# Performance work log

Measured on AMD Instinct MI355X. Metric: run time of the kernel, lower is better.

Reference implementation:

```python
import jax, jax.numpy as jnp
import numpy as np

HID = 512
HEADS = 8
HEAD_DIM = HID // HEADS
B, S = 2, 4096


def setup_inputs() -> dict:
    key = jax.random.key(0)
    ks = jax.random.split(key, 11)
    sc = 0.02
    return {
        "query": jax.random.normal(ks[0], (B, S, HID), jnp.float32),
        "key": jax.random.normal(ks[1], (B, S, HID), jnp.float32),
        "value": jax.random.normal(ks[2], (B, S, HID), jnp.float32),
        "Wq": jax.random.normal(ks[3], (HID, HID), jnp.float32) * sc,
        "bq": jax.random.normal(ks[4], (HID,), jnp.float32) * sc,
        "Wk": jax.random.normal(ks[5], (HID, HID), jnp.float32) * sc,
        "bk": jax.random.normal(ks[6], (HID,), jnp.float32) * sc,
        "Wv": jax.random.normal(ks[7], (HID, HID), jnp.float32) * sc,
        "bv": jax.random.normal(ks[8], (HID,), jnp.float32) * sc,
        "Wo": jax.random.normal(ks[9], (HID, HID), jnp.float32) * sc,
        "bo": jax.random.normal(ks[10], (HID,), jnp.float32) * sc,
    }


def reference(query, key, value, Wq, bq, Wk, bk, Wv, bv, Wo, bo):
    b, s, _ = query.shape
    scale = jnp.sqrt(jnp.float32(HEAD_DIM))
    # projections (nn.Linear: x @ W.T + b)
    Q = query @ Wq.T + bq
    K = key @ Wk.T + bk
    V = value @ Wv.T + bv
    # split heads: [b, h, s, d]
    Q = Q.reshape(b, s, HEADS, HEAD_DIM).transpose(0, 2, 1, 3)
    K = K.reshape(b, s, HEADS, HEAD_DIM).transpose(0, 2, 1, 3)
    V = V.reshape(b, s, HEADS, HEAD_DIM).transpose(0, 2, 1, 3)
    # scaled dot-product attention (mask=None, dropout in eval mode = identity)
    energy = jnp.einsum('bhqd,bhkd->bhqk', Q, K) / scale
    attention = jax.nn.softmax(energy, axis=-1)
    x = jnp.einsum('bhqk,bhkd->bhqd', attention, V)
    x = x.transpose(0, 2, 1, 3).reshape(b, s, HID)
    return x @ Wo.T + bo
```

## Files before the change

kernel.cpp:

```cpp
#include <hip/hip_runtime.h>
#include <stdint.h>

#define HID 512
#define NH 8
#define HD 64
#define BATCH 2
#define SEQ 4096
#define M_TOT (BATCH*SEQ)
#define NBH (BATCH*NH)
#define SPLITK 4

typedef __attribute__((ext_vector_type(8))) short short8;
typedef __attribute__((ext_vector_type(4))) float floatx4;
typedef unsigned short u16;

__device__ inline u16 f2bf(float x) {
  unsigned u = __builtin_bit_cast(unsigned, x);
  unsigned r = u + 0x7fff + ((u >> 16) & 1);
  return (u16)(r >> 16);
}

__device__ inline float bf2f(u16 h) {
  unsigned u = ((unsigned)h) << 16;
  return __builtin_bit_cast(float, u);
}

__device__ inline unsigned cvt_pk_bf16(float a, float b) {
  unsigned r;
  asm("v_cvt_pk_bf16_f32 %0, %1, %2" : "=v"(r) : "v"(a), "v"(b));
  return r;
}

__device__ inline void gll16(const void* g, void* l) {
  __builtin_amdgcn_global_load_lds((const __attribute__((address_space(1))) void*)g,
                                   (__attribute__((address_space(3))) void*)l, 16, 0, 0);
}


__global__ void cvt_all(const float* __restrict__ q, const float* __restrict__ k,
                        const float* __restrict__ v, const float* __restrict__ wq,
                        const float* __restrict__ wk, const float* __restrict__ wv,
                        const float* __restrict__ wo,
                        u16* __restrict__ xq, u16* __restrict__ xk,
                        u16* __restrict__ xv, u16* __restrict__ wb) {
  const size_t NW = (size_t)HID * HID;
  int bx = (int)blockIdx.x;
  const float* src; u16* dst; int blk;
  if (bx < 12288) {
    int seg = bx >> 12;
    blk = bx & 4095;
    src = (seg == 0) ? q : ((seg == 1) ? k : v);
    dst = (seg == 0) ? xq : ((seg == 1) ? xk : xv);
  } else {
    int w = (bx - 12288) >> 8;
    blk = (bx - 12288) & 255;
    src = (w == 0) ? wq : ((w == 1) ? wk : ((w == 2) ? wv : wo));
    dst = wb + (size_t)w * NW;
  }
  int i = (blk * 256 + (int)threadIdx.x) * 4;
  const float4 val = *(const float4*)(src + i);
  union { uint2 u; u16 h[4]; } pk;
  pk.h[0] = f2bf(val.x); pk.h[1] = f2bf(val.y);
  pk.h[2] = f2bf(val.z); pk.h[3] = f2bf(val.w);
  *(uint2*)(dst + i) = pk.u;
}

__global__ __launch_bounds__(256) void gemm_qkv(
    const u16* __restrict__ Xq, const u16* __restrict__ Xk, const u16* __restrict__ Xv,
    const u16* __restrict__ Wb,
    const float* __restrict__ bq, const float* __restrict__ bk, const float* __restrict__ bv,
    u16* __restrict__ Qp, u16* __restrict__ Kp, u16* __restrict__ Vt) {
  const int z = blockIdx.z;
  const u16* X = (z == 0) ? Xq : ((z == 1) ? Xk : Xv);
  const u16* W = Wb + (size_t)z * (HID * HID);
  const float* bias = (z == 0) ? bq : ((z == 1) ? bk : bv);

  __shared__ u16 As[128 * 32];
  __shared__ u16 Bs[128 * 32];

  const int tid = threadIdx.x;
  const int wid = tid >> 6, lane = tid & 63;
  const int wm = wid >> 1, wn = wid & 1;
  const int quad = lane >> 4, l16 = lane & 15;
  const int m0 = (int)blockIdx.x * 128, n0 = (int)blockIdx.y * 128;
  const int srow = lane >> 2;
  const int scol = (lane & 3) * 8;

  floatx4 acc[4][4];
#pragma unroll
  for (int i = 0; i < 4; i++)
#pragma unroll
    for (int j = 0; j < 4; j++) acc[i][j] = floatx4{0.f, 0.f, 0.f, 0.f};

  for (int k0 = 0; k0 < HID; k0 += 32) {
#pragma unroll
    for (int r = 0; r < 2; r++) {
      int row = r * 64 + wid * 16 + srow;
      gll16(X + (size_t)(m0 + row) * HID + k0 + scol, &As[(r * 64 + wid * 16) * 32]);
      gll16(W + (size_t)(n0 + row) * HID + k0 + scol, &Bs[(r * 64 + wid * 16) * 32]);
    }
    __syncthreads();
    short8 af[4], bf[4];
#pragma unroll
    for (int mt = 0; mt < 4; mt++)
      af[mt] = *(const short8*)&As[(wm * 64 + mt * 16 + l16) * 32 + quad * 8];
#pragma unroll
    for (int nt = 0; nt < 4; nt++)
      bf[nt] = *(const short8*)&Bs[(wn * 64 + nt * 16 + l16) * 32 + quad * 8];
#pragma unroll
    for (int mt = 0; mt < 4; mt++)
#pragma unroll
      for (int nt = 0; nt < 4; nt++)
        acc[mt][nt] = __builtin_amdgcn_mfma_f32_16x16x32_bf16(af[mt], bf[nt], acc[mt][nt], 0, 0, 0);
    __syncthreads();
  }

#pragma unroll
  for (int mt = 0; mt < 4; mt++) {
#pragma unroll
    for (int nt = 0; nt < 4; nt++) {
      int ncol = n0 + wn * 64 + nt * 16 + l16;
      float bias_v = bias[ncol];
      int h = ncol >> 6, d = ncol & 63;
#pragma unroll
      for (int r = 0; r < 4; r++) {
        int mrow = m0 + wm * 64 + mt * 16 + quad * 4 + r;
        float v = acc[mt][nt][r] + bias_v;
        int b = mrow >> 12, s = mrow & (SEQ - 1);
        size_t base = (size_t)(b * NH + h) * SEQ * HD;
        if (z == 2) {
          int kk = ((s >> 2) & 3) * 8 + ((s >> 4) & 1) * 4 + (s & 3);
          size_t idx = base + (size_t)(s >> 5) * 2048 + (d >> 4) * 512
                     + (kk >> 3) * 128 + (d & 15) * 8 + (kk & 7);
          Vt[idx] = f2bf(v);
        } else {
          size_t idx = base + (size_t)(s >> 4) * 1024 + (d >> 3) * 128 + (s & 15) * 8 + (d & 7);
          if (z == 0) Qp[idx] = f2bf(v * 0.18033688f);
          else        Kp[idx] = f2bf(v);
        }
      }
    }
  }
}

__global__ __launch_bounds__(256) void gemm_out(
    const u16* __restrict__ X, const u16* __restrict__ W,
    const float* __restrict__ bias, float* __restrict__ out) {
  __shared__ u16 As[128 * 32];
  __shared__ u16 Bs[64 * 32];

  const int tid = threadIdx.x;
  const int wid = tid >> 6, lane = tid & 63;
  const int wm = wid >> 1, wn = wid & 1;
  const int quad = lane >> 4, l16 = lane & 15;
  const int m0 = (int)blockIdx.x * 128, n0 = (int)blockIdx.y * 64;
  const int srow = lane >> 2;
  const int scol = (lane & 3) * 8;

  floatx4 acc[4][2];
#pragma unroll
  for (int i = 0; i < 4; i++)
#pragma unroll
    for (int j = 0; j < 2; j++) acc[i][j] = floatx4{0.f, 0.f, 0.f, 0.f};

  for (int k0 = 0; k0 < HID; k0 += 32) {
#pragma unroll
    for (int r = 0; r < 2; r++) {
      int row = r * 64 + wid * 16 + srow;
      gll16(X + (size_t)(m0 + row) * HID + k0 + scol, &As[(r * 64 + wid * 16) * 32]);
    }
    {
      int row = wid * 16 + srow;
      gll16(W + (size_t)(n0 + row) * HID + k0 + scol, &Bs[(wid * 16) * 32]);
    }
    __syncthreads();
    short8 af[4], bf[2];
#pragma unroll
    for (int mt = 0; mt < 4; mt++)
      af[mt] = *(const short8*)&As[(wm * 64 + mt * 16 + l16) * 32 + quad * 8];
#pragma unroll
    for (int nt = 0; nt < 2; nt++)
      bf[nt] = *(const short8*)&Bs[(wn * 32 + nt * 16 + l16) * 32 + quad * 8];
#pragma unroll
    for (int mt = 0; mt < 4; mt++)
#pragma unroll
      for (int nt = 0; nt < 2; nt++)
        acc[mt][nt] = __builtin_amdgcn_mfma_f32_16x16x32_bf16(af[mt], bf[nt], acc[mt][nt], 0, 0, 0);
    __syncthreads();
  }

#pragma unroll
  for (int mt = 0; mt < 4; mt++) {
#pragma unroll
    for (int nt = 0; nt < 2; nt++) {
      int ncol = n0 + wn * 32 + nt * 16 + l16;
      float bias_v = bias[ncol];
#pragma unroll
      for (int r = 0; r < 4; r++) {
        int mrow = m0 + wm * 64 + mt * 16 + quad * 4 + r;
        out[(size_t)mrow * HID + ncol] = acc[mt][nt][r] + bias_v;
      }
    }
  }
}

__global__ __launch_bounds__(256) void attn_kernel(
    const u16* __restrict__ Qp, const u16* __restrict__ Kp,
    const u16* __restrict__ Vt, u16* __restrict__ Opb, float* __restrict__ Lp) {
  const int bh = blockIdx.y;
  const int sp = blockIdx.z;
  const int q0 = (int)blockIdx.x * 128;
  const u16* Qh = Qp + (size_t)bh * SEQ * HD;
  const u16* Kh = Kp + (size_t)bh * SEQ * HD;
  const u16* Vh = Vt + (size_t)bh * SEQ * HD;

  __shared__ u16 Ks[2][4096];
  __shared__ u16 Vs[2][4096];

  const int tid = threadIdx.x;
  const int wid = tid >> 6, lane = tid & 63;
  const int quad = lane >> 4, l16 = lane & 15;

  short8 qf[2][2];
#pragma unroll
  for (int kq = 0; kq < 2; kq++)
#pragma unroll
    for (int n = 0; n < 2; n++)
      qf[kq][n] = *(const short8*)(Qh + (size_t)(q0 / 16 + wid * 2 + n) * 1024 + (kq * 4 + quad) * 128 + l16 * 8);

  float l_part[2] = {0.f, 0.f};
  floatx4 o[2][4];
#pragma unroll
  for (int m = 0; m < 2; m++)
#pragma unroll
    for (int dt = 0; dt < 4; dt++) o[m][dt] = floatx4{0.f, 0.f, 0.f, 0.f};

  const int kv_lo = sp * (SEQ / SPLITK), kv_hi = kv_lo + SEQ / SPLITK;

  auto stage = [&](int buf, int kv0) {
    const u16* kg = Kh + (size_t)(kv0 >> 4) * 1024;
    const u16* vg = Vh + (size_t)(kv0 >> 4) * 1024;
#pragma unroll
    for (int r = 0; r < 2; r++) {
      int c = wid + r * 4;
      gll16(kg + c * 512 + lane * 8, &Ks[buf][c * 512]);
      gll16(vg + c * 512 + lane * 8, &Vs[buf][c * 512]);
    }
  };

  stage(0, kv_lo);
  __syncthreads();

  int ibuf = 0;
  for (int kv0 = kv_lo; kv0 < kv_hi; kv0 += 64) {
    if (kv0 + 64 < kv_hi) stage(ibuf ^ 1, kv0 + 64);

#pragma unroll
    for (int gg = 0; gg < 2; gg++) {
      const u16* Kb = &Ks[ibuf][gg * 2048];
      short8 akA0 = *(const short8*)&Kb[quad * 128 + l16 * 8];
      short8 akA1 = *(const short8*)&Kb[(4 + quad) * 128 + l16 * 8];
      short8 akB0 = *(const short8*)&Kb[1024 + quad * 128 + l16 * 8];
      short8 akB1 = *(const short8*)&Kb[1024 + (4 + quad) * 128 + l16 * 8];
      short8 vf[4];
#pragma unroll
      for (int dt = 0; dt < 4; dt++)
        vf[dt] = *(const short8*)&Vs[ibuf][gg * 2048 + dt * 512 + quad * 128 + l16 * 8];

      floatx4 stA[2], stB[2];
#pragma unroll
      for (int n = 0; n < 2; n++) {
        stA[n] = __builtin_amdgcn_mfma_f32_16x16x32_bf16(akA0, qf[0][n], floatx4{0.f,0.f,0.f,0.f}, 0, 0, 0);
        stB[n] = __builtin_amdgcn_mfma_f32_16x16x32_bf16(akB0, qf[0][n], floatx4{0.f,0.f,0.f,0.f}, 0, 0, 0);
        stA[n] = __builtin_amdgcn_mfma_f32_16x16x32_bf16(akA1, qf[1][n], stA[n], 0, 0, 0);
        stB[n] = __builtin_amdgcn_mfma_f32_16x16x32_bf16(akB1, qf[1][n], stB[n], 0, 0, 0);
      }

#pragma unroll
      for (int n = 0; n < 2; n++) {
        float a0 = __builtin_amdgcn_exp2f(stA[n][0]);
        float a1 = __builtin_amdgcn_exp2f(stA[n][1]);
        float a2 = __builtin_amdgcn_exp2f(stA[n][2]);
        float a3 = __builtin_amdgcn_exp2f(stA[n][3]);
        float b0 = __builtin_amdgcn_exp2f(stB[n][0]);
        float b1 = __builtin_amdgcn_exp2f(stB[n][1]);
        float b2 = __builtin_amdgcn_exp2f(stB[n][2]);
        float b3 = __builtin_amdgcn_exp2f(stB[n][3]);
        l_part[n] += ((a0 + a1) + (a2 + a3)) + ((b0 + b1) + (b2 + b3));
        union { unsigned u[4]; short8 s; } pk;
        pk.u[0] = cvt_pk_bf16(a0, a1);
        pk.u[1] = cvt_pk_bf16(a2, a3);
        pk.u[2] = cvt_pk_bf16(b0, b1);
        pk.u[3] = cvt_pk_bf16(b2, b3);
#pragma unroll
        for (int dt = 0; dt < 4; dt++)
          o[n][dt] = __builtin_amdgcn_mfma_f32_16x16x32_bf16(pk.s, vf[dt], o[n][dt], 0, 0, 0);
      }
    }
    __syncthreads();
    ibuf ^= 1;
  }

#pragma unroll
  for (int n = 0; n < 2; n++) {
    l_part[n] += __shfl_xor(l_part[n], 16);
    l_part[n] += __shfl_xor(l_part[n], 32);
  }
  u16* Oph = Opb + (size_t)(sp * NBH + bh) * SEQ * HD;
  float* Lph = Lp + (size_t)(sp * NBH + bh) * SEQ;
  if (quad == 0) {
#pragma unroll
    for (int n = 0; n < 2; n++)
      Lph[q0 + wid * 32 + n * 16 + l16] = l_part[n];
  }
#pragma unroll
  for (int m = 0; m < 2; m++) {
#pragma unroll
    for (int r = 0; r < 4; r++) {
      int s = q0 + wid * 32 + m * 16 + quad * 4 + r;
#pragma unroll
      for (int dt = 0; dt < 4; dt++)
        Oph[(size_t)s * HD + dt * 16 + l16] = f2bf(o[m][dt][r]);
    }
  }
}

__global__ __launch_bounds__(256) void combine_kernel(
    const u16* __restrict__ Opb, const float* __restrict__ Lp, u16* __restrict__ Xo) {
  int idx = (int)blockIdx.x * 256 + (int)threadIdx.x;
  int e = idx * 4;
  int bh = e >> 18;
  int rem = e & 262143;
  int q = rem >> 6, d = rem & 63;
  float acc0 = 0.f, acc1 = 0.f, acc2 = 0.f, acc3 = 0.f, lsum = 0.f;
#pragma unroll
  for (int sp = 0; sp < SPLITK; sp++) {
    size_t i = ((size_t)(sp * NBH + bh) * SEQ + q) * HD + d;
    union { uint2 u; u16 h[4]; } pk;
    pk.u = *(const uint2*)(Opb + i);
    acc0 += bf2f(pk.h[0]); acc1 += bf2f(pk.h[1]);
    acc2 += bf2f(pk.h[2]); acc3 += bf2f(pk.h[3]);
    lsum += Lp[(size_t)(sp * NBH + bh) * SEQ + q];
  }
  float inv = 1.f / lsum;
  int b = bh >> 3, h = bh & 7;
  u16* dst = Xo + ((size_t)(b * SEQ + q)) * HID + h * HD + d;
  union { uint2 u; u16 hh[4]; } pk;
  pk.hh[0] = f2bf(acc0 * inv);
  pk.hh[1] = f2bf(acc1 * inv);
  pk.hh[2] = f2bf(acc2 * inv);
  pk.hh[3] = f2bf(acc3 * inv);
  *(uint2*)dst = pk.u;
}

extern "C" void kernel_launch(void* const* d_in, const int* in_sizes, int n_in,
                              void* d_out, int out_size, void* d_ws, size_t ws_size,
                              hipStream_t stream) {
  const float* q  = (const float*)d_in[0];
  const float* k  = (const float*)d_in[1];
  const float* v  = (const float*)d_in[2];
  const float* Wq = (const float*)d_in[3];
  const float* bq = (const float*)d_in[4];
  const float* Wk = (const float*)d_in[5];
  const float* bk = (const float*)d_in[6];
  const float* Wv = (const float*)d_in[7];
  const float* bv = (const float*)d_in[8];
  const float* Wo = (const float*)d_in[9];
  const float* bo = (const float*)d_in[10];

  u16* wsb = (u16*)d_ws;
  const size_t NW = (size_t)HID * HID;
  const size_t NX = (size_t)M_TOT * HID;
  u16* Wb = wsb;
  u16* Xq = wsb + 4 * NW;
  u16* Xk = Xq + NX;
  u16* Xv = Xk + NX;
  u16* Qp = Xv + NX;
  u16* Kp = Qp + NX;
  u16* Vt = Kp + NX;
  u16* Xo = Vt + NX;
  u16* Opb = Xo + NX;
  float* Lp = (float*)(Opb + (size_t)SPLITK * NBH * SEQ * HD);

  dim3 blk(256);
  cvt_all<<<dim3(13312), blk, 0, stream>>>(q, k, v, Wq, Wk, Wv, Wo, Xq, Xk, Xv, Wb);

  gemm_qkv<<<dim3(64, 4, 3), blk, 0, stream>>>(Xq, Xk, Xv, Wb, bq, bk, bv, Qp, Kp, Vt);
  attn_kernel<<<dim3(32, NBH, SPLITK), blk, 0, stream>>>(Qp, Kp, Vt, Opb, Lp);
  combine_kernel<<<dim3(4096), blk, 0, stream>>>(Opb, Lp, Xo);
  gemm_out<<<dim3(64, 8), blk, 0, stream>>>(Xo, Wb + 3 * NW, bo, (float*)d_out);
}
```

Measured before the change: 234.3 us.

## Fuse activation bf16 conversion into QKV GEMM and split-K combine into output GEMM

The fp32 activations are no longer converted to bf16 in a separate pass. Instead the QKV GEMM loads fp32 rows and packs them to bf16 while writing LDS. The separate combine kernel is also removed: the output projection GEMM sums the split-K partial outputs and normalizes them by the summed softmax denominators while staging its A tile. This saves two launches and several full-size intermediate reads and writes. In exchange, the GEMM A-loads become synchronous register loads, and gemm_out re-reads the four partials once for each of its 8 column blocks.

```diff
diff --git a/kernel.cpp b/kernel.cpp
--- a/kernel.cpp
+++ b/kernel.cpp
@@ -37,26 +37,15 @@
 }
 
 
-__global__ void cvt_all(const float* __restrict__ q, const float* __restrict__ k,
-                        const float* __restrict__ v, const float* __restrict__ wq,
-                        const float* __restrict__ wk, const float* __restrict__ wv,
-                        const float* __restrict__ wo,
-                        u16* __restrict__ xq, u16* __restrict__ xk,
-                        u16* __restrict__ xv, u16* __restrict__ wb) {
+__global__ void cvt_w(const float* __restrict__ wq, const float* __restrict__ wk,
+                      const float* __restrict__ wv, const float* __restrict__ wo,
+                      u16* __restrict__ wb) {
   const size_t NW = (size_t)HID * HID;
   int bx = (int)blockIdx.x;
-  const float* src; u16* dst; int blk;
-  if (bx < 12288) {
-    int seg = bx >> 12;
-    blk = bx & 4095;
-    src = (seg == 0) ? q : ((seg == 1) ? k : v);
-    dst = (seg == 0) ? xq : ((seg == 1) ? xk : xv);
-  } else {
-    int w = (bx - 12288) >> 8;
-    blk = (bx - 12288) & 255;
-    src = (w == 0) ? wq : ((w == 1) ? wk : ((w == 2) ? wv : wo));
-    dst = wb + (size_t)w * NW;
-  }
+  int w = bx >> 8;
+  int blk = bx & 255;
+  const float* src = (w == 0) ? wq : ((w == 1) ? wk : ((w == 2) ? wv : wo));
+  u16* dst = wb + (size_t)w * NW;
   int i = (blk * 256 + (int)threadIdx.x) * 4;
   const float4 val = *(const float4*)(src + i);
   union { uint2 u; u16 h[4]; } pk;
@@ -66,12 +55,12 @@
 }
 
 __global__ __launch_bounds__(256) void gemm_qkv(
-    const u16* __restrict__ Xq, const u16* __restrict__ Xk, const u16* __restrict__ Xv,
+    const float* __restrict__ Xq, const float* __restrict__ Xk, const float* __restrict__ Xv,
     const u16* __restrict__ Wb,
     const float* __restrict__ bq, const float* __restrict__ bk, const float* __restrict__ bv,
     u16* __restrict__ Qp, u16* __restrict__ Kp, u16* __restrict__ Vt) {
   const int z = blockIdx.z;
-  const u16* X = (z == 0) ? Xq : ((z == 1) ? Xk : Xv);
+  const float* X = (z == 0) ? Xq : ((z == 1) ? Xk : Xv);
   const u16* W = Wb + (size_t)z * (HID * HID);
   const float* bias = (z == 0) ? bq : ((z == 1) ? bk : bv);
 
@@ -96,7 +85,15 @@
 #pragma unroll
     for (int r = 0; r < 2; r++) {
       int row = r * 64 + wid * 16 + srow;
-      gll16(X + (size_t)(m0 + row) * HID + k0 + scol, &As[(r * 64 + wid * 16) * 32]);
+      const float* srcp = X + (size_t)(m0 + row) * HID + k0 + scol;
+      float4 p0 = *(const float4*)srcp;
+      float4 p1 = *(const float4*)(srcp + 4);
+      union { unsigned u[4]; short8 s; } pka;
+      pka.u[0] = cvt_pk_bf16(p0.x, p0.y);
+      pka.u[1] = cvt_pk_bf16(p0.z, p0.w);
+      pka.u[2] = cvt_pk_bf16(p1.x, p1.y);
+      pka.u[3] = cvt_pk_bf16(p1.z, p1.w);
+      *(short8*)&As[(r * 64 + wid * 16) * 32 + lane * 8] = pka.s;
       gll16(W + (size_t)(n0 + row) * HID + k0 + scol, &Bs[(r * 64 + wid * 16) * 32]);
     }
     __syncthreads();
@@ -144,7 +141,8 @@
 }
 
 __global__ __launch_bounds__(256) void gemm_out(
-    const u16* __restrict__ X, const u16* __restrict__ W,
+    const u16* __restrict__ Opb, const float* __restrict__ Lp,
+    const u16* __restrict__ W,
     const float* __restrict__ bias, float* __restrict__ out) {
   __shared__ u16 As[128 * 32];
   __shared__ u16 Bs[64 * 32];
@@ -157,35 +155,72 @@
   const int srow = lane >> 2;
   const int scol = (lane & 3) * 8;
 
+  float invl[2][NH];
+#pragma unroll
+  for (int r = 0; r < 2; r++) {
+    int mrow = m0 + r * 64 + wid * 16 + srow;
+    int b = mrow >> 12, qq = mrow & (SEQ - 1);
+#pragma unroll
+    for (int h = 0; h < NH; h++) {
+      float s = 0.f;
+#pragma unroll
+      for (int sp = 0; sp < SPLITK; sp++)
+        s += Lp[(size_t)(sp * NBH + b * NH + h) * SEQ + qq];
+      invl[r][h] = 1.f / s;
+    }
+  }
+
   floatx4 acc[4][2];
 #pragma unroll
   for (int i = 0; i < 4; i++)
 #pragma unroll
     for (int j = 0; j < 2; j++) acc[i][j] = floatx4{0.f, 0.f, 0.f, 0.f};
 
-  for (int k0 = 0; k0 < HID; k0 += 32) {
+#pragma unroll
+  for (int kb = 0; kb < 16; kb++) {
+    const int k0 = kb * 32;
+    const int h = k0 >> 6;
+    const int d = (k0 + scol) & 63;
 #pragma unroll
     for (int r = 0; r < 2; r++) {
-      int row = r * 64 + wid * 16 + srow;
-      gll16(X + (size_t)(m0 + row) * HID + k0 + scol, &As[(r * 64 + wid * 16) * 32]);
+      int mrow = m0 + r * 64 + wid * 16 + srow;
+      int b = mrow >> 12, qq = mrow & (SEQ - 1);
+      int bh = b * NH + h;
+      float a0 = 0.f, a1 = 0.f, a2 = 0.f, a3 = 0.f, a4 = 0.f, a5 = 0.f, a6 = 0.f, a7 = 0.f;
+#pragma unroll
+      for (int sp = 0; sp < SPLITK; sp++) {
+        const u16* p = Opb + ((size_t)(sp * NBH + bh) * SEQ + qq) * HD + d;
+        short8 vv = *(const short8*)p;
+        a0 += bf2f((u16)vv[0]); a1 += bf2f((u16)vv[1]);
+        a2 += bf2f((u16)vv[2]); a3 += bf2f((u16)vv[3]);
+        a4 += bf2f((u16)vv[4]); a5 += bf2f((u16)vv[5]);
+        a6 += bf2f((u16)vv[6]); a7 += bf2f((u16)vv[7]);
+      }
+      float inv = invl[r][h];
+      union { unsigned u[4]; short8 s; } pka;
+      pka.u[0] = cvt_pk_bf16(a0 * inv, a1 * inv);
+      pka.u[1] = cvt_pk_bf16(a2 * inv, a3 * inv);
+      pka.u[2] = cvt_pk_bf16(a4 * inv, a5 * inv);
+      pka.u[3] = cvt_pk_bf16(a6 * inv, a7 * inv);
+      *(short8*)&As[(r * 64 + wid * 16) * 32 + lane * 8] = pka.s;
     }
     {
       int row = wid * 16 + srow;
       gll16(W + (size_t)(n0 + row) * HID + k0 + scol, &Bs[(wid * 16) * 32]);
     }
     __syncthreads();
-    short8 af[4], bf[2];
+    short8 af[4], bfr[2];
 #pragma unroll
     for (int mt = 0; mt < 4; mt++)
       af[mt] = *(const short8*)&As[(wm * 64 + mt * 16 + l16) * 32 + quad * 8];
 #pragma unroll
     for (int nt = 0; nt < 2; nt++)
-      bf[nt] = *(const short8*)&Bs[(wn * 32 + nt * 16 + l16) * 32 + quad * 8];
+      bfr[nt] = *(const short8*)&Bs[(wn * 32 + nt * 16 + l16) * 32 + quad * 8];
 #pragma unroll
     for (int mt = 0; mt < 4; mt++)
 #pragma unroll
       for (int nt = 0; nt < 2; nt++)
-        acc[mt][nt] = __builtin_amdgcn_mfma_f32_16x16x32_bf16(af[mt], bf[nt], acc[mt][nt], 0, 0, 0);
+        acc[mt][nt] = __builtin_amdgcn_mfma_f32_16x16x32_bf16(af[mt], bfr[nt], acc[mt][nt], 0, 0, 0);
     __syncthreads();
   }
 
@@ -325,34 +360,6 @@
   }
 }
 
-__global__ __launch_bounds__(256) void combine_kernel(
-    const u16* __restrict__ Opb, const float* __restrict__ Lp, u16* __restrict__ Xo) {
-  int idx = (int)blockIdx.x * 256 + (int)threadIdx.x;
-  int e = idx * 4;
-  int bh = e >> 18;
-  int rem = e & 262143;
-  int q = rem >> 6, d = rem & 63;
-  float acc0 = 0.f, acc1 = 0.f, acc2 = 0.f, acc3 = 0.f, lsum = 0.f;
-#pragma unroll
-  for (int sp = 0; sp < SPLITK; sp++) {
-    size_t i = ((size_t)(sp * NBH + bh) * SEQ + q) * HD + d;
-    union { uint2 u; u16 h[4]; } pk;
-    pk.u = *(const uint2*)(Opb + i);
-    acc0 += bf2f(pk.h[0]); acc1 += bf2f(pk.h[1]);
-    acc2 += bf2f(pk.h[2]); acc3 += bf2f(pk.h[3]);
-    lsum += Lp[(size_t)(sp * NBH + bh) * SEQ + q];
-  }
-  float inv = 1.f / lsum;
-  int b = bh >> 3, h = bh & 7;
-  u16* dst = Xo + ((size_t)(b * SEQ + q)) * HID + h * HD + d;
-  union { uint2 u; u16 hh[4]; } pk;
-  pk.hh[0] = f2bf(acc0 * inv);
-  pk.hh[1] = f2bf(acc1 * inv);
-  pk.hh[2] = f2bf(acc2 * inv);
-  pk.hh[3] = f2bf(acc3 * inv);
-  *(uint2*)dst = pk.u;
-}
-
 extern "C" void kernel_launch(void* const* d_in, const int* in_sizes, int n_in,
                               void* d_out, int out_size, void* d_ws, size_t ws_size,
                               hipStream_t stream) {
@@ -372,21 +379,15 @@
   const size_t NW = (size_t)HID * HID;
   const size_t NX = (size_t)M_TOT * HID;
   u16* Wb = wsb;
-  u16* Xq = wsb + 4 * NW;
-  u16* Xk = Xq + NX;
-  u16* Xv = Xk + NX;
-  u16* Qp = Xv + NX;
+  u16* Qp = wsb + 4 * NW;
   u16* Kp = Qp + NX;
   u16* Vt = Kp + NX;
-  u16* Xo = Vt + NX;
-  u16* Opb = Xo + NX;
+  u16* Opb = Vt + NX;
   float* Lp = (float*)(Opb + (size_t)SPLITK * NBH * SEQ * HD);
 
   dim3 blk(256);
-  cvt_all<<<dim3(13312), blk, 0, stream>>>(q, k, v, Wq, Wk, Wv, Wo, Xq, Xk, Xv, Wb);
-
-  gemm_qkv<<<dim3(64, 4, 3), blk, 0, stream>>>(Xq, Xk, Xv, Wb, bq, bk, bv, Qp, Kp, Vt);
+  cvt_w<<<dim3(1024), blk, 0, stream>>>(Wq, Wk, Wv, Wo, Wb);
+  gemm_qkv<<<dim3(64, 4, 3), blk, 0, stream>>>(q, k, v, Wb, bq, bk, bv, Qp, Kp, Vt);
   attn_kernel<<<dim3(32, NBH, SPLITK), blk, 0, stream>>>(Qp, Kp, Vt, Opb, Lp);
-  combine_kernel<<<dim3(4096), blk, 0, stream>>>(Opb, Lp, Xo);
-  gemm_out<<<dim3(64, 8), blk, 0, stream>>>(Xo, Wb + 3 * NW, bo, (float*)d_out);
-}
+  gemm_out<<<dim3(64, 8), blk, 0, stream>>>(Opb, Lp, Wb + 3 * NW, bo, (float*)d_out);
+}
```

After: 240.6 us. +2.7%, slower.
